# Kernel tuning notes

Hardware: AMD Instinct MI355X
Metric: run time of the kernel (lower is better)

The kernel has to match this reference:

```python
import math
import jax, jax.numpy as jnp
import numpy as np

H = 12          # num_attention_heads
D = 128         # head_dim = 1536 // 12
E = H * D       # hidden_size
CHUNK = 12      # attention_chunk_size
PAST = 12       # attention_context_left - 1
FUT = 0         # attention_context_right
CTX = CHUNK + PAST + FUT   # 24
CAP = 50.0      # attention_logit_cap
Q_SCALE = D ** (-0.5) / math.log(2.0)
K_SCALE = math.log(1.0 + math.e) / math.log(2.0)


def setup_inputs() -> dict:
    key = jax.random.key(0)
    ks = jax.random.split(key, 8)
    B, S = 8, 3072
    w_scale = E ** (-0.5)
    return {
        "hidden_states": jax.random.normal(ks[0], (B, S, E), jnp.float32),
        "position_embeddings": jax.random.normal(ks[1], (CTX, E), jnp.float32),
        "w_q": jax.random.normal(ks[2], (E, E), jnp.float32) * w_scale,
        "w_k": jax.random.normal(ks[3], (E, E), jnp.float32) * w_scale,
        "w_v": jax.random.normal(ks[4], (E, E), jnp.float32) * w_scale,
        "w_post": jax.random.normal(ks[5], (E, E), jnp.float32) * w_scale,
        "w_rel": jax.random.normal(ks[6], (E, E), jnp.float32) * w_scale,
        "per_dim_scale": jnp.zeros((D,), jnp.float32),
    }


def _rel_shift(x):
    # x: [B, H, nb, chunk, P] with P <= CTX+1 -> [B, H, nb, chunk, CTX]
    B, h, nb, bs, p = x.shape
    x = jnp.pad(x, ((0, 0), (0, 0), (0, 0), (0, 0), (0, CTX + 1 - p)))
    x = x.reshape(B, h, nb, bs * (CTX + 1))[..., : bs * CTX]
    return x.reshape(B, h, nb, bs, CTX)


def reference(hidden_states, position_embeddings, w_q, w_k, w_v, w_post, w_rel, per_dim_scale):
    B, S, _ = hidden_states.shape
    # projections (torch Linear: y = x @ W.T), computed in float32
    q = (hidden_states @ w_q.T).reshape(B, S, H, D)
    k = (hidden_states @ w_k.T).reshape(B, S, H, D)
    v = (hidden_states @ w_v.T).reshape(B, S, H, D)
    q = q * (Q_SCALE * jax.nn.softplus(per_dim_scale))  # per-dim query scale
    k = k * K_SCALE

    nb = (S + CHUNK - 1) // CHUNK
    pad = nb * CHUNK - S
    # convert_to_block: [B, nb, CHUNK, H, D]
    qb = jnp.pad(q, ((0, 0), (0, pad), (0, 0), (0, 0))).reshape(B, nb, CHUNK, H, D)

    def ctx_extract(x):
        # pad left by PAST, right by FUT + CHUNK - 1, then gather CTX-wide windows strided by CHUNK
        xp = jnp.pad(x, ((0, 0), (PAST, FUT + CHUNK - 1), (0, 0), (0, 0)))
        idx = jnp.arange(nb)[:, None] * CHUNK + jnp.arange(CTX)[None, :]
        return xp[:, idx]  # [B, nb, CTX, H, D]

    kc = ctx_extract(k)
    vc = ctx_extract(v)

    rel_k = (position_embeddings @ w_rel.T).reshape(-1, H, D)  # [P, H, D]

    # content term: [B, H, nb, CHUNK, CTX]
    ac = jnp.einsum('bnchd,bnkhd->bhnck', qb, kc)
    # position term + Transformer-XL rel shift
    bd = jnp.einsum('bnchd,phd->bhncp', qb, rel_k)
    bd = _rel_shift(bd)

    logits = ac + bd
    logits = jnp.tanh(logits / CAP) * CAP  # softcap
    attn_weights = jax.nn.softmax(logits, axis=-1)

    out = jnp.einsum('bhnck,bnkhd->bnchd', attn_weights, vc)
    out = out.reshape(B, nb * CHUNK, H * D)[:, :S]
    out = out @ w_post.T
    return out, attn_weights
```

## Files before the change

kernel.cpp:

```cpp
#include <hip/hip_runtime.h>
#include <hip/hip_bf16.h>

#define HH 12
#define DD 128
#define EE 1536
#define QKVP 4608
#define NBATCH 8
#define SEQ 3072
#define NBLK 256
#define CHK 12
#define CTXW 24
#define MTOK 24576

#define Q_SCALE_BASE 0.12751743f
#define K_SCALE_F 1.8946361322f

#define PITCH 65

typedef short s16x8 __attribute__((ext_vector_type(8)));
typedef float f32x4 __attribute__((ext_vector_type(4)));

__device__ __forceinline__ float bf2f(unsigned short u) {
  return __builtin_bit_cast(float, ((unsigned int)u) << 16);
}
__device__ __forceinline__ unsigned short f2bf(float f) {
  unsigned int u = __builtin_bit_cast(unsigned int, f);
  u += 0x7fffu + ((u >> 16) & 1u);
  return (unsigned short)(u >> 16);
}
__device__ __forceinline__ void bf2f2(unsigned int u, float& lo, float& hi) {
  lo = __builtin_bit_cast(float, u << 16);
  hi = __builtin_bit_cast(float, u & 0xffff0000u);
}

__device__ __forceinline__ void async16(const void* g, void* l) {
  __builtin_amdgcn_global_load_lds(
      (const __attribute__((address_space(1))) unsigned int*)g,
      (__attribute__((address_space(3))) unsigned int*)l, 16, 0, 0);
}

__global__ __launch_bounds__(256) void k_cvt(const float4* __restrict__ in,
                                             ushort4* __restrict__ out, int n4) {
  int i = blockIdx.x * 256 + threadIdx.x;
  if (i < n4) {
    float4 v = in[i];
    ushort4 o;
    o.x = f2bf(v.x); o.y = f2bf(v.y); o.z = f2bf(v.z); o.w = f2bf(v.w);
    out[i] = o;
  }
}

__global__ void k_qscale(const float* __restrict__ pds, float* __restrict__ qs) {
  int d = threadIdx.x;
  if (d < DD) {
    float x = pds[d];
    float sp = (x > 20.f) ? x : log1pf(expf(x));
    qs[d] = Q_SCALE_BASE * sp;
  }
}

__global__ __launch_bounds__(256) void k_rel(const float* __restrict__ pos,
                                             const float* __restrict__ w_rel,
                                             unsigned short* __restrict__ rel16) {
  __shared__ unsigned short lp[12 * EE];
  const int t = threadIdx.x;
  const int p0 = blockIdx.y * 12;
  for (int i = t; i < 12 * EE / 4; i += 256) {
    float4 x = ((const float4*)(pos + (long)p0 * EE))[i];
    ushort4 o; o.x = f2bf(x.x); o.y = f2bf(x.y); o.z = f2bf(x.z); o.w = f2bf(x.w);
    ((ushort4*)lp)[i] = o;
  }
  __syncthreads();
  const int col = blockIdx.x * 128 + (t & 127);
  const int pg = t >> 7;
  float acc[6] = {0.f, 0.f, 0.f, 0.f, 0.f, 0.f};
  const float* wr = w_rel + (long)col * EE;
  for (int e = 0; e < EE; ++e) {
    float w = wr[e];
#pragma unroll
    for (int i = 0; i < 6; ++i) acc[i] += w * bf2f(lp[(pg * 6 + i) * EE + e]);
  }
#pragma unroll
  for (int i = 0; i < 6; ++i)
    rel16[(long)(p0 + pg * 6 + i) * EE + col] = f2bf(acc[i]);
}


__device__ __forceinline__ void stage_half(const unsigned short* g0, long Kl,
                                           unsigned short* lhalf,
                                           int w, int rlo, int qz) {
  const unsigned short* s0 = g0 + (long)(w * 16 + rlo) * Kl + qz * 8;
  async16(s0,          lhalf + w * 1024);
  async16(s0 + 8 * Kl, lhalf + w * 1024 + 512);
}

__device__ __forceinline__ void tile4(
    unsigned short* AP, unsigned short* BP,
    unsigned short* AQ, unsigned short* BQ,
    const unsigned short* gAt, const unsigned short* gBt, long Kl,
    int t1, int t2, int w, int rlo, int qz,
    int aBase, int bBase, int sw0, int sw1, f32x4 (&acc)[8][4]) {
  s16x8 af[4], bf[4];

#pragma unroll
  for (int i = 0; i < 4; ++i) af[i] = *(const s16x8*)&AP[(aBase + 16 * i) * 64 + sw0];
#pragma unroll
  for (int j = 0; j < 4; ++j) bf[j] = *(const s16x8*)&BP[(bBase + 16 * j) * 64 + sw0];
  stage_half(gBt + 128 * Kl + (long)t1 * 64, Kl, BQ + 8192, w, rlo, qz);
  __builtin_amdgcn_s_barrier();
  __builtin_amdgcn_s_setprio(1);
#pragma unroll
  for (int i = 0; i < 4; ++i)
#pragma unroll
    for (int j = 0; j < 4; ++j)
      acc[i][j] = __builtin_amdgcn_mfma_f32_16x16x32_bf16(af[i], bf[j], acc[i][j], 0, 0, 0);
  __builtin_amdgcn_s_setprio(0);
  __builtin_amdgcn_s_barrier();

#pragma unroll
  for (int i = 0; i < 4; ++i) af[i] = *(const s16x8*)&AP[(aBase + 64 + 16 * i) * 64 + sw0];
  stage_half(gAt + (long)t1 * 64, Kl, AQ, w, rlo, qz);
  __builtin_amdgcn_s_barrier();
  __builtin_amdgcn_s_setprio(1);
#pragma unroll
  for (int i = 0; i < 4; ++i)
#pragma unroll
    for (int j = 0; j < 4; ++j)
      acc[4 + i][j] = __builtin_amdgcn_mfma_f32_16x16x32_bf16(af[i], bf[j], acc[4 + i][j], 0, 0, 0);
  __builtin_amdgcn_s_setprio(0);
  __builtin_amdgcn_s_barrier();

#pragma unroll
  for (int i = 0; i < 4; ++i) af[i] = *(const s16x8*)&AP[(aBase + 16 * i) * 64 + sw1];
#pragma unroll
  for (int j = 0; j < 4; ++j) bf[j] = *(const s16x8*)&BP[(bBase + 16 * j) * 64 + sw1];
  stage_half(gAt + 128 * Kl + (long)t1 * 64, Kl, AQ + 8192, w, rlo, qz);
  __builtin_amdgcn_s_barrier();
  __builtin_amdgcn_s_setprio(1);
#pragma unroll
  for (int i = 0; i < 4; ++i)
#pragma unroll
    for (int j = 0; j < 4; ++j)
      acc[i][j] = __builtin_amdgcn_mfma_f32_16x16x32_bf16(af[i], bf[j], acc[i][j], 0, 0, 0);
  __builtin_amdgcn_s_setprio(0);
  __builtin_amdgcn_s_barrier();

#pragma unroll
  for (int i = 0; i < 4; ++i) af[i] = *(const s16x8*)&AP[(aBase + 64 + 16 * i) * 64 + sw1];
  stage_half(gBt + (long)t2 * 64, Kl, BP, w, rlo, qz);
  asm volatile("s_waitcnt vmcnt(2)" ::: "memory");
  __builtin_amdgcn_s_barrier();
  __builtin_amdgcn_s_setprio(1);
#pragma unroll
  for (int i = 0; i < 4; ++i)
#pragma unroll
    for (int j = 0; j < 4; ++j)
      acc[4 + i][j] = __builtin_amdgcn_mfma_f32_16x16x32_bf16(af[i], bf[j], acc[4 + i][j], 0, 0, 0);
  __builtin_amdgcn_s_setprio(0);
  __builtin_amdgcn_s_barrier();
}

__global__ __launch_bounds__(512, 2) void k_gemm256(
    const unsigned short* __restrict__ A, const unsigned short* __restrict__ Bt,
    void* __restrict__ Cv, int M, int N, int K, int gN,
    int mode, const float* __restrict__ qscale, int c_f32) {
  __shared__ unsigned short sm[65536];

  const int tid = threadIdx.x;
  const int w = tid >> 6;
  const int lane = tid & 63;
  const int quad = lane >> 4;
  const int l16 = lane & 15;
  const int sw = l16 & 7;
  const int rlo = lane >> 3;
  const int qz = (lane & 7) ^ rlo;

  const int nwg = gridDim.x;
  const int orig = blockIdx.x;
  const int qd = nwg >> 3;
  const int wg = (orig & 7) * qd + (orig >> 3);
  const int mt = wg / gN, nt = wg - mt * gN;
  const long bm = (long)mt * 256, bn = (long)nt * 256;
  const long Kl = K;
  const unsigned short* gAt = A + bm * Kl;
  const unsigned short* gBt = Bt + bn * Kl;

  unsigned short* A0 = sm;
  unsigned short* B0 = sm + 16384;
  unsigned short* A1 = sm + 32768;
  unsigned short* B1 = sm + 49152;

  const int aBase = (w >> 2) * 128 + l16;
  const int bBase = (w & 3) * 64 + l16;
  const int sw0 = ((quad ^ sw) & 7) * 8;
  const int sw1 = (((4 | quad) ^ sw) & 7) * 8;

  f32x4 acc[8][4] = {};
  const int NT = K >> 6;

  stage_half(gBt,            Kl, B0,        w, rlo, qz);
  stage_half(gBt + 128 * Kl, Kl, B0 + 8192, w, rlo, qz);
  stage_half(gAt,            Kl, A0,        w, rlo, qz);
  stage_half(gAt + 128 * Kl, Kl, A0 + 8192, w, rlo, qz);
  stage_half(gBt + 64,       Kl, B1,        w, rlo, qz);
  asm volatile("s_waitcnt vmcnt(2)" ::: "memory");
  __builtin_amdgcn_s_barrier();

  for (int t = 0; t < NT; t += 2) {
    const int t2 = (t + 2 == NT) ? 0 : t + 2;
    const int u2 = (t + 3 >= NT) ? t + 3 - NT : t + 3;
    tile4(A0, B0, A1, B1, gAt, gBt, Kl, t + 1, t2, w, rlo, qz, aBase, bBase, sw0, sw1, acc);
    tile4(A1, B1, A0, B0, gAt, gBt, Kl, t2,    u2, w, rlo, qz, aBase, bBase, sw0, sw1, acc);
  }

  const int wmq = (w >> 2) * 128;
  const int wnq = (w & 3) * 64;
#pragma unroll
  for (int j = 0; j < 4; ++j) {
    const long col = bn + wnq + 16 * j + l16;
    float scale = 1.0f;
    if (mode == 3)
      scale = (col < 1536) ? qscale[col & (DD - 1)] : (col < 3072 ? K_SCALE_F : 1.0f);
#pragma unroll
    for (int i = 0; i < 8; ++i) {
      const long row0 = bm + wmq + 16 * i + quad * 4;
#pragma unroll
      for (int r = 0; r < 4; ++r) {
        float vv = acc[i][j][r] * scale;
        if (c_f32) ((float*)Cv)[(row0 + r) * (long)N + col] = vv;
        else ((unsigned short*)Cv)[(row0 + r) * (long)N + col] = f2bf(vv);
      }
    }
  }
}

__global__ __launch_bounds__(256) void k_attn(
    const unsigned short* __restrict__ qkv, const unsigned short* __restrict__ rel,
    unsigned short* __restrict__ attn_out, float* __restrict__ aw_out) {
  const int n = blockIdx.x;
  const int b = blockIdx.y;
  const int h = blockIdx.z;
  const int t = threadIdx.x;

  __shared__ unsigned int lq[CHK * PITCH];
  __shared__ unsigned int lk[CTXW * PITCH];
  __shared__ unsigned int lv[CTXW * PITCH];
  __shared__ unsigned int lr[CTXW * PITCH];
  __shared__ float sac[CHK * CTXW];
  __shared__ float sbd[CHK * CTXW];
  __shared__ float smax[CHK];
  __shared__ float sinv[CHK];

  const long tok0 = (long)b * SEQ + (long)n * CHK;
  const long hq = (long)h * DD;

  for (int u = t; u < CHK * 16; u += 256) {
    int r = u >> 4, w4 = u & 15;
    uint4 x = *(const uint4*)&qkv[(tok0 + r) * QKVP + hq + w4 * 8];
    unsigned int* d = &lq[r * PITCH + w4 * 4];
    d[0] = x.x; d[1] = x.y; d[2] = x.z; d[3] = x.w;
  }
  for (int u = t; u < CTXW * 16; u += 256) {
    int r = u >> 4, w4 = u & 15;
    int s = n * CHK + r - 12;
    uint4 kx, vx;
    if (s >= 0) {
      const unsigned short* base = &qkv[((long)b * SEQ + s) * QKVP + hq];
      kx = *(const uint4*)&base[1536 + w4 * 8];
      vx = *(const uint4*)&base[3072 + w4 * 8];
    } else {
      kx = make_uint4(0, 0, 0, 0);
      vx = make_uint4(0, 0, 0, 0);
    }
    uint4 rx = *(const uint4*)&rel[(long)r * EE + hq + w4 * 8];
    unsigned int* dk = &lk[r * PITCH + w4 * 4];
    unsigned int* dv = &lv[r * PITCH + w4 * 4];
    unsigned int* dr = &lr[r * PITCH + w4 * 4];
    dk[0] = kx.x; dk[1] = kx.y; dk[2] = kx.z; dk[3] = kx.w;
    dv[0] = vx.x; dv[1] = vx.y; dv[2] = vx.z; dv[3] = vx.w;
    dr[0] = rx.x; dr[1] = rx.y; dr[2] = rx.z; dr[3] = rx.w;
  }
  __syncthreads();

  for (int p = t; p < CHK * CTXW; p += 256) {
    int c = p / CTXW, j = p - c * CTXW;
    const unsigned int* uq = &lq[c * PITCH];
    const unsigned int* uk = &lk[j * PITCH];
    const unsigned int* ur = &lr[j * PITCH];
    float ac = 0.f, bd = 0.f;
#pragma unroll 16
    for (int d2 = 0; d2 < DD / 2; ++d2) {
      float a0, a1, k0f, k1f, r0, r1;
      bf2f2(uq[d2], a0, a1);
      bf2f2(uk[d2], k0f, k1f);
      bf2f2(ur[d2], r0, r1);
      ac += a0 * k0f + a1 * k1f;
      bd += a0 * r0 + a1 * r1;
    }
    sac[p] = ac;
    sbd[p] = bd;
  }
  __syncthreads();

  for (int p = t; p < CHK * CTXW; p += 256) {
    int c = p / CTXW, j = p - c * CTXW;
    float y;
    if (j >= c) y = sbd[c * CTXW + (j - c)];
    else if (j == c - 1) y = 0.f;
    else y = sbd[(c - 1) * CTXW + (j - c + CTXW + 1)];
    float x = (sac[p] + y) * 0.02f;
    x = fminf(fmaxf(x, -15.f), 15.f);
    float e2 = __expf(2.f * x);
    sac[p] = 50.f * (e2 - 1.f) / (e2 + 1.f);
  }
  __syncthreads();

  if (t < CHK) {
    float m = -3.0e38f;
#pragma unroll
    for (int j = 0; j < CTXW; ++j) m = fmaxf(m, sac[t * CTXW + j]);
    smax[t] = m;
  }
  __syncthreads();

  for (int p = t; p < CHK * CTXW; p += 256) {
    int c = p / CTXW;
    sbd[p] = __expf(sac[p] - smax[c]);
  }
  __syncthreads();

  if (t < CHK) {
    float s = 0.f;
#pragma unroll
    for (int j = 0; j < CTXW; ++j) s += sbd[t * CTXW + j];
    sinv[t] = 1.f / s;
  }
  __syncthreads();

  for (int p = t; p < CHK * CTXW; p += 256) {
    int c = p / CTXW, j = p - c * CTXW;
    float w = sbd[p] * sinv[c];
    sac[p] = w;
    aw_out[((((long)b * HH + h) * NBLK + n) * CHK + c) * CTXW + j] = w;
  }
  __syncthreads();

  for (int p = t; p < CHK * (DD / 2); p += 256) {
    int c = p >> 6, d2 = p & 63;
    float a0 = 0.f, a1 = 0.f;
#pragma unroll
    for (int j = 0; j < CTXW; ++j) {
      float w = sac[c * CTXW + j];
      float v0, v1;
      bf2f2(lv[j * PITCH + d2], v0, v1);
      a0 += w * v0; a1 += w * v1;
    }
    unsigned int packed = ((unsigned int)f2bf(a1) << 16) | (unsigned int)f2bf(a0);
    *(unsigned int*)&attn_out[(tok0 + c) * EE + hq + d2 * 2] = packed;
  }
}

extern "C" void kernel_launch(void* const* d_in, const int* in_sizes, int n_in,
                              void* d_out, int out_size, void* d_ws, size_t ws_size,
                              hipStream_t stream) {
  const float* hs     = (const float*)d_in[0];
  const float* pos    = (const float*)d_in[1];
  const float* w_q    = (const float*)d_in[2];
  const float* w_k    = (const float*)d_in[3];
  const float* w_v    = (const float*)d_in[4];
  const float* w_post = (const float*)d_in[5];
  const float* w_rel  = (const float*)d_in[6];
  const float* pds    = (const float*)d_in[7];

  char* ws = (char*)d_ws;
  const size_t TOKB = (size_t)MTOK * EE * 2;
  const size_t WB   = (size_t)EE * EE * 2;
  unsigned short* hs16   = (unsigned short*)(ws);
  unsigned short* qkv16  = (unsigned short*)(ws + TOKB);
  unsigned short* wq16   = (unsigned short*)(ws + 4 * TOKB);
  unsigned short* wk16   = (unsigned short*)(ws + 4 * TOKB + WB);
  unsigned short* wv16   = (unsigned short*)(ws + 4 * TOKB + 2 * WB);
  unsigned short* wp16   = (unsigned short*)(ws + 4 * TOKB + 3 * WB);
  unsigned short* rel16  = (unsigned short*)(ws + 4 * TOKB + 4 * WB);
  float* qscale          = (float*)(ws + 4 * TOKB + 4 * WB + CTXW * EE * 2);
  unsigned short* attn16 = hs16;

  float* out = (float*)d_out;
  float* aw  = out + (size_t)MTOK * EE;

  k_cvt<<<36864, 256, 0, stream>>>((const float4*)hs, (ushort4*)hs16, MTOK * EE / 4);
  k_cvt<<<2304, 256, 0, stream>>>((const float4*)w_q, (ushort4*)wq16, EE * EE / 4);
  k_cvt<<<2304, 256, 0, stream>>>((const float4*)w_k, (ushort4*)wk16, EE * EE / 4);
  k_cvt<<<2304, 256, 0, stream>>>((const float4*)w_v, (ushort4*)wv16, EE * EE / 4);
  k_cvt<<<2304, 256, 0, stream>>>((const float4*)w_post, (ushort4*)wp16, EE * EE / 4);
  k_qscale<<<1, 128, 0, stream>>>(pds, qscale);
  k_rel<<<dim3(12, 2), 256, 0, stream>>>(pos, w_rel, rel16);

  k_gemm256<<<dim3((MTOK / 256) * (QKVP / 256)), 512, 0, stream>>>(
      hs16, wq16, qkv16, MTOK, QKVP, EE, QKVP / 256, 3, qscale, 0);

  k_attn<<<dim3(NBLK, NBATCH, HH), 256, 0, stream>>>(qkv16, rel16, attn16, aw);

  k_gemm256<<<dim3((MTOK / 256) * (EE / 256)), 512, 0, stream>>>(
      attn16, wp16, out, MTOK, EE, EE, EE / 256, 0, nullptr, 1);
}
```

Before: 1.119 ms.

## Stage GEMM epilogue through LDS, rework prefetch order and tile rasterization

```diff
diff --git a/kernel.cpp b/kernel.cpp
--- a/kernel.cpp
+++ b/kernel.cpp
@@ -106,7 +106,7 @@
   for (int i = 0; i < 4; ++i) af[i] = *(const s16x8*)&AP[(aBase + 16 * i) * 64 + sw0];
 #pragma unroll
   for (int j = 0; j < 4; ++j) bf[j] = *(const s16x8*)&BP[(bBase + 16 * j) * 64 + sw0];
-  stage_half(gBt + 128 * Kl + (long)t1 * 64, Kl, BQ + 8192, w, rlo, qz);
+  stage_half(gAt + (long)t1 * 64, Kl, AQ, w, rlo, qz);
   __builtin_amdgcn_s_barrier();
   __builtin_amdgcn_s_setprio(1);
 #pragma unroll
@@ -119,7 +119,7 @@
 
 #pragma unroll
   for (int i = 0; i < 4; ++i) af[i] = *(const s16x8*)&AP[(aBase + 64 + 16 * i) * 64 + sw0];
-  stage_half(gAt + (long)t1 * 64, Kl, AQ, w, rlo, qz);
+  stage_half(gAt + 128 * Kl + (long)t1 * 64, Kl, AQ + 8192, w, rlo, qz);
   __builtin_amdgcn_s_barrier();
   __builtin_amdgcn_s_setprio(1);
 #pragma unroll
@@ -134,7 +134,6 @@
   for (int i = 0; i < 4; ++i) af[i] = *(const s16x8*)&AP[(aBase + 16 * i) * 64 + sw1];
 #pragma unroll
   for (int j = 0; j < 4; ++j) bf[j] = *(const s16x8*)&BP[(bBase + 16 * j) * 64 + sw1];
-  stage_half(gAt + 128 * Kl + (long)t1 * 64, Kl, AQ + 8192, w, rlo, qz);
   __builtin_amdgcn_s_barrier();
   __builtin_amdgcn_s_setprio(1);
 #pragma unroll
@@ -148,7 +147,8 @@
 #pragma unroll
   for (int i = 0; i < 4; ++i) af[i] = *(const s16x8*)&AP[(aBase + 64 + 16 * i) * 64 + sw1];
   stage_half(gBt + (long)t2 * 64, Kl, BP, w, rlo, qz);
-  asm volatile("s_waitcnt vmcnt(2)" ::: "memory");
+  stage_half(gBt + 128 * Kl + (long)t2 * 64, Kl, BP + 8192, w, rlo, qz);
+  asm volatile("s_waitcnt vmcnt(4)" ::: "memory");
   __builtin_amdgcn_s_barrier();
   __builtin_amdgcn_s_setprio(1);
 #pragma unroll
@@ -178,8 +178,16 @@
   const int nwg = gridDim.x;
   const int orig = blockIdx.x;
   const int qd = nwg >> 3;
-  const int wg = (orig & 7) * qd + (orig >> 3);
-  const int mt = wg / gN, nt = wg - mt * gN;
+  const int xcd = orig & 7;
+  const int u = orig >> 3;
+  const int bandsz = 4 * gN;
+  const int band = u / bandsz;
+  const int rem = u - band * bandsz;
+  const int mi = band * 4 + (rem & 3);
+  const int ni = rem >> 2;
+  const int mloc = qd / gN;
+  const int mt = xcd * mloc + mi;
+  const int nt = ni;
   const long bm = (long)mt * 256, bn = (long)nt * 256;
   const long Kl = K;
   const unsigned short* gAt = A + bm * Kl;
@@ -198,38 +206,90 @@
   f32x4 acc[8][4] = {};
   const int NT = K >> 6;
 
+  stage_half(gAt,            Kl, A0,        w, rlo, qz);
+  stage_half(gAt + 128 * Kl, Kl, A0 + 8192, w, rlo, qz);
   stage_half(gBt,            Kl, B0,        w, rlo, qz);
   stage_half(gBt + 128 * Kl, Kl, B0 + 8192, w, rlo, qz);
-  stage_half(gAt,            Kl, A0,        w, rlo, qz);
-  stage_half(gAt + 128 * Kl, Kl, A0 + 8192, w, rlo, qz);
-  stage_half(gBt + 64,       Kl, B1,        w, rlo, qz);
-  asm volatile("s_waitcnt vmcnt(2)" ::: "memory");
+  stage_half(gBt + 64,            Kl, B1,        w, rlo, qz);
+  stage_half(gBt + 128 * Kl + 64, Kl, B1 + 8192, w, rlo, qz);
+  asm volatile("s_waitcnt vmcnt(4)" ::: "memory");
   __builtin_amdgcn_s_barrier();
 
   for (int t = 0; t < NT; t += 2) {
+    const int t1 = t + 1;
     const int t2 = (t + 2 == NT) ? 0 : t + 2;
-    const int u2 = (t + 3 >= NT) ? t + 3 - NT : t + 3;
-    tile4(A0, B0, A1, B1, gAt, gBt, Kl, t + 1, t2, w, rlo, qz, aBase, bBase, sw0, sw1, acc);
-    tile4(A1, B1, A0, B0, gAt, gBt, Kl, t2,    u2, w, rlo, qz, aBase, bBase, sw0, sw1, acc);
-  }
+    const int t3 = (t + 3 >= NT) ? t + 3 - NT : t + 3;
+    tile4(A0, B0, A1, B1, gAt, gBt, Kl, t1, t2, w, rlo, qz, aBase, bBase, sw0, sw1, acc);
+    tile4(A1, B1, A0, B0, gAt, gBt, Kl, t2, t3, w, rlo, qz, aBase, bBase, sw0, sw1, acc);
+  }
+
+  __syncthreads();
 
   const int wmq = (w >> 2) * 128;
   const int wnq = (w & 3) * 64;
-#pragma unroll
-  for (int j = 0; j < 4; ++j) {
-    const long col = bn + wnq + 16 * j + l16;
-    float scale = 1.0f;
-    if (mode == 3)
-      scale = (col < 1536) ? qscale[col & (DD - 1)] : (col < 3072 ? K_SCALE_F : 1.0f);
-#pragma unroll
-    for (int i = 0; i < 8; ++i) {
-      const long row0 = bm + wmq + 16 * i + quad * 4;
-#pragma unroll
-      for (int r = 0; r < 4; ++r) {
-        float vv = acc[i][j][r] * scale;
-        if (c_f32) ((float*)Cv)[(row0 + r) * (long)N + col] = vv;
-        else ((unsigned short*)Cv)[(row0 + r) * (long)N + col] = f2bf(vv);
+
+  if (!c_f32) {
+#pragma unroll
+    for (int j = 0; j < 4; ++j) {
+      const long col = bn + wnq + 16 * j + l16;
+      float scale = 1.0f;
+      if (mode == 3)
+        scale = (col < 1536) ? qscale[col & (DD - 1)] : (col < 3072 ? K_SCALE_F : 1.0f);
+      const int lc = wnq + 16 * j + l16;
+#pragma unroll
+      for (int i = 0; i < 8; ++i) {
+        const int lr0 = wmq + 16 * i + quad * 4;
+#pragma unroll
+        for (int r = 0; r < 4; ++r) {
+          const int lr = lr0 + r;
+          const int gsw = (lc >> 3) ^ ((lr >> 2) & 7);
+          sm[lr * 256 + gsw * 8 + (lc & 7)] = f2bf(acc[i][j][r] * scale);
+        }
       }
+    }
+    __syncthreads();
+#pragma unroll
+    for (int k = 0; k < 16; ++k) {
+      const int G = k * 512 + tid;
+      const int row = G >> 5, gc = G & 31;
+      const int gsw = gc ^ ((row >> 2) & 7);
+      s16x8 vdat = *(const s16x8*)&sm[row * 256 + gsw * 8];
+      *(s16x8*)&((unsigned short*)Cv)[(bm + row) * (long)N + bn + gc * 8] = vdat;
+    }
+  } else {
+    float* Cf = (float*)sm;
+#pragma unroll
+    for (int h = 0; h < 2; ++h) {
+      if ((wmq == 0) == (h == 0)) {
+#pragma unroll
+        for (int j = 0; j < 4; ++j) {
+          const long col = bn + wnq + 16 * j + l16;
+          float scale = 1.0f;
+          if (mode == 3)
+            scale = (col < 1536) ? qscale[col & (DD - 1)] : (col < 3072 ? K_SCALE_F : 1.0f);
+          const int lc = wnq + 16 * j + l16;
+#pragma unroll
+          for (int i = 0; i < 8; ++i) {
+            const int lr0 = 16 * i + quad * 4;
+#pragma unroll
+            for (int r = 0; r < 4; ++r) {
+              const int lr = lr0 + r;
+              const int gsw = (lc >> 2) ^ ((lr >> 2) & 7);
+              Cf[lr * 256 + gsw * 4 + (lc & 3)] = acc[i][j][r] * scale;
+            }
+          }
+        }
+      }
+      __syncthreads();
+#pragma unroll
+      for (int k = 0; k < 16; ++k) {
+        const int G = k * 512 + tid;
+        const int row = G >> 6, gc = G & 63;
+        const int gsw = gc ^ ((row >> 2) & 7);
+        float4 vdat = *(const float4*)&Cf[row * 256 + gsw * 4];
+        *(float4*)&((float*)Cv)[(bm + h * 128 + row) * (long)N + bn + gc * 4] = vdat;
+      }
+      __syncthreads();
     }
   }
 }
```

Result: faster. 1.033 ms (-7.7%).
